# Performance work log

Measured on AMD Instinct MI355X. Metric: run time of the kernel, lower is better.

## Reference

```python
import jax, jax.numpy as jnp
import numpy as np

B, N, E = 16, 1024, 32768
HEADS, OC = 4, 8          # GATConv: out_channels = d_out // heads = 8
D_IN, A_DIM = 33, 8
DM, DO = 16, 32
EPS_LN = 1e-5


def setup_inputs() -> dict:
    key = jax.random.key(0)
    ks = jax.random.split(key, 24)
    r = lambda k, s: (0.1 * jax.random.normal(k, s)).astype(jnp.float32)
    return {
        "H": jax.random.normal(ks[0], (B, N, D_IN + A_DIM + 1), dtype=jnp.float32),
        "edge_index": jax.random.randint(ks[1], (2, E), 0, N, dtype=jnp.int32),
        "fc_s_w": r(ks[2], (DM, D_IN)), "fc_s_b": r(ks[3], (DM,)),
        "fc_a_w": r(ks[4], (DM, A_DIM)), "fc_a_b": r(ks[5], (DM,)),
        "fc_r_w": r(ks[6], (DM, 1)), "fc_r_b": r(ks[7], (DM,)),
        "fuse_q": r(ks[8], (3, DM)),
        "fuse_k_w": r(ks[9], (DM, DM)),
        "fuse_v_w": r(ks[10], (DM, DM)),
        "proj_w": r(ks[11], (DO, DM)), "proj_b": r(ks[12], (DO,)),
        "post_w": r(ks[13], (DO, DO)), "post_b": r(ks[14], (DO,)),
        "ln_g": jnp.ones((DO,), jnp.float32), "ln_b": jnp.zeros((DO,), jnp.float32),
        "gat_w": r(ks[15], (HEADS * OC, DO)),
        "att_src": r(ks[16], (HEADS, OC)),
        "att_dst": r(ks[17], (HEADS, OC)),
        "gat_b": r(ks[18], (HEADS * OC,)),
    }


def reference(H, edge_index, fc_s_w, fc_s_b, fc_a_w, fc_a_b, fc_r_w, fc_r_b,
              fuse_q, fuse_k_w, fuse_v_w, proj_w, proj_b, post_w, post_b,
              ln_g, ln_b, gat_w, att_src, att_dst, gat_b):
    # ---- ObsEmbedding: split obs | prev-action | prev-reward, embed to DM ----
    s = H[..., :D_IN]
    a = H[..., D_IN:D_IN + A_DIM]
    rr = H[..., D_IN + A_DIM:]
    tok = jnp.stack([s @ fc_s_w.T + fc_s_b,
                     a @ fc_a_w.T + fc_a_b,
                     rr @ fc_r_w.T + fc_r_b], axis=-2)            # [B,N,3,DM]
    K = tok @ fuse_k_w.T
    V = tok @ fuse_v_w.T
    attn = jnp.einsum('qd,bntd->bnqt', fuse_q, K) / jnp.sqrt(jnp.float32(DM))
    w = jax.nn.softmax(attn, axis=-1)                             # [B,N,3,3]
    fused = jnp.einsum('bnqt,bntd->bnqd', w, V).mean(-2)          # [B,N,DM]
    z = jax.nn.relu(fused) @ proj_w.T + proj_b                    # [B,N,DO]
    h = jax.nn.relu(z @ post_w.T + post_b)
    mu = h.mean(-1, keepdims=True)
    var = ((h - mu) ** 2).mean(-1, keepdims=True)
    Hn = (h - mu) / jnp.sqrt(var + EPS_LN) * ln_g + ln_b          # [B,N,DO]

    # ---- GATConv (eval mode: dropout off, add_self_loops=False) ----
    src, dst = edge_index[0], edge_index[1]
    x = (Hn @ gat_w.T).reshape(B, N, HEADS, OC)                   # [B,N,H,OC]
    a_s = (x * att_src).sum(-1)                                   # [B,N,H]
    a_d = (x * att_dst).sum(-1)
    e = jax.nn.leaky_relu(a_s[:, src] + a_d[:, dst], 0.2)         # [B,E,H]

    def per_graph(e_b, x_b):
        # scatter-softmax over incoming edges of each destination node
        m = jax.ops.segment_max(e_b, dst, num_segments=N)
        ex = jnp.exp(e_b - m[dst])
        den = jax.ops.segment_sum(ex, dst, num_segments=N)
        alpha = ex / den[dst]                                     # [E,H]
        out = jax.ops.segment_sum(alpha[:, :, None] * x_b[src], dst,
                                  num_segments=N)                 # [N,H,OC]
        A = jnp.zeros((HEADS, N, N), jnp.float32).at[:, src, dst].add(alpha.T)
        A = A / jnp.maximum(A.sum(-1, keepdims=True), 1e-9)
        return out.reshape(N, HEADS * OC) + gat_b, A

    out, A = jax.vmap(per_graph)(e, x)                            # [B,N,32], [B,H,N,N]
    return out, A
```

## Files before the change

### kernel.cpp

```cpp
#include <hip/hip_runtime.h>
#include <math.h>

namespace {

constexpr int B = 16, N = 1024, E = 32768, HEADS = 4, OC = 8;
constexpr int D_IN = 33, A_DIM = 8, DM = 16, DO = 32;
constexpr int F = D_IN + A_DIM + 1;
constexpr int CAP = 128;
constexpr int BCAP = 256;

typedef float f4 __attribute__((ext_vector_type(4)));

__device__ __forceinline__ float lrelu(float x) { return x >= 0.f ? x : 0.2f * x; }

__global__ __launch_bounds__(64) void k_node(
    const float* __restrict__ H,
    const float* __restrict__ fc_s_w, const float* __restrict__ fc_s_b,
    const float* __restrict__ fc_a_w, const float* __restrict__ fc_a_b,
    const float* __restrict__ fc_r_w, const float* __restrict__ fc_r_b,
    const float* __restrict__ fuse_q, const float* __restrict__ fuse_k_w,
    const float* __restrict__ fuse_v_w, const float* __restrict__ proj_w,
    const float* __restrict__ proj_b, const float* __restrict__ post_w,
    const float* __restrict__ post_b, const float* __restrict__ ln_g,
    const float* __restrict__ ln_b, const float* __restrict__ gat_w,
    const float* __restrict__ att_src, const float* __restrict__ att_dst,
    float* __restrict__ x_out, float* __restrict__ as_out, float* __restrict__ advi) {
  int node = blockIdx.x * blockDim.x + threadIdx.x;
  if (node >= B * N) return;

  const float* hin = H + (size_t)node * F;
  float hv[F];
#pragma unroll
  for (int i = 0; i < F; i++) hv[i] = hin[i];

  float tok[3][DM];
#pragma unroll
  for (int j = 0; j < DM; j++) {
    float acc = fc_s_b[j];
#pragma unroll
    for (int i = 0; i < D_IN; i++) acc = fmaf(hv[i], fc_s_w[j * D_IN + i], acc);
    tok[0][j] = acc;
    float acc2 = fc_a_b[j];
#pragma unroll
    for (int i = 0; i < A_DIM; i++) acc2 = fmaf(hv[D_IN + i], fc_a_w[j * A_DIM + i], acc2);
    tok[1][j] = acc2;
    tok[2][j] = fmaf(hv[F - 1], fc_r_w[j], fc_r_b[j]);
  }

  float Kf[3][DM], Vf[3][DM];
#pragma unroll
  for (int t = 0; t < 3; t++) {
#pragma unroll
    for (int j = 0; j < DM; j++) {
      float ak = 0.f, av = 0.f;
#pragma unroll
      for (int d = 0; d < DM; d++) {
        ak = fmaf(tok[t][d], fuse_k_w[j * DM + d], ak);
        av = fmaf(tok[t][d], fuse_v_w[j * DM + d], av);
      }
      Kf[t][j] = ak; Vf[t][j] = av;
    }
  }

  float wbar[3] = {0.f, 0.f, 0.f};
#pragma unroll
  for (int q = 0; q < 3; q++) {
    float att[3];
#pragma unroll
    for (int t = 0; t < 3; t++) {
      float acc = 0.f;
#pragma unroll
      for (int d = 0; d < DM; d++) acc = fmaf(fuse_q[q * DM + d], Kf[t][d], acc);
      att[t] = acc * 0.25f;
    }
    float mx = fmaxf(att[0], fmaxf(att[1], att[2]));
    float e0 = expf(att[0] - mx), e1 = expf(att[1] - mx), e2 = expf(att[2] - mx);
    float inv = 1.f / (e0 + e1 + e2);
    wbar[0] += e0 * inv; wbar[1] += e1 * inv; wbar[2] += e2 * inv;
  }

  float fused[DM];
#pragma unroll
  for (int d = 0; d < DM; d++) {
    float f = (wbar[0] * Vf[0][d] + wbar[1] * Vf[1][d] + wbar[2] * Vf[2][d]) * (1.f / 3.f);
    fused[d] = fmaxf(f, 0.f);
  }

  float z[DO];
#pragma unroll
  for (int o = 0; o < DO; o++) {
    float acc = proj_b[o];
#pragma unroll
    for (int d = 0; d < DM; d++) acc = fmaf(fused[d], proj_w[o * DM + d], acc);
    z[o] = acc;
  }

  float h2[DO]; float mu = 0.f;
#pragma unroll
  for (int o = 0; o < DO; o++) {
    float acc = post_b[o];
#pragma unroll
    for (int d = 0; d < DO; d++) acc = fmaf(z[d], post_w[o * DO + d], acc);
    acc = fmaxf(acc, 0.f);
    h2[o] = acc; mu += acc;
  }
  mu *= (1.f / DO);
  float var = 0.f;
#pragma unroll
  for (int o = 0; o < DO; o++) { float dd = h2[o] - mu; var = fmaf(dd, dd, var); }
  var *= (1.f / DO);
  float rstd = rsqrtf(var + 1e-5f);
  float Hn[DO];
#pragma unroll
  for (int o = 0; o < DO; o++) Hn[o] = fmaf((h2[o] - mu) * rstd, ln_g[o], ln_b[o]);

  float* xrow = x_out + (size_t)node * (HEADS * OC);
  f4 asv, adv;
#pragma unroll
  for (int hh = 0; hh < HEADS; hh++) {
    float as = 0.f, ad = 0.f;
#pragma unroll
    for (int oc = 0; oc < OC; oc++) {
      int k = hh * OC + oc;
      float acc = 0.f;
#pragma unroll
      for (int d = 0; d < DO; d++) acc = fmaf(Hn[d], gat_w[k * DO + d], acc);
      xrow[k] = acc;
      as = fmaf(acc, att_src[k], as);
      ad = fmaf(acc, att_dst[k], ad);
    }
    asv[hh] = as; adv[hh] = ad;
  }
  *(f4*)(as_out + (size_t)node * HEADS) = asv;
  *(f4*)(advi + (size_t)node * 8) = adv;
}

__global__ void k_fill(const int* __restrict__ ei, int* __restrict__ cnt_src,
                       int* __restrict__ cnt_dst, int* __restrict__ bkt_src,
                       int* __restrict__ bkt_dst) {
  int e = blockIdx.x * blockDim.x + threadIdx.x;
  if (e >= E) return;
  int s = ei[e], d = ei[E + e];
  int p1 = atomicAdd(&cnt_src[s], 1);
  if (p1 < BCAP) bkt_src[s * BCAP + p1] = d;
  int p2 = atomicAdd(&cnt_dst[d], 1);
  if (p2 < BCAP) bkt_dst[d * BCAP + p2] = s;
}

__global__ __launch_bounds__(256) void k_dst(
    const int* __restrict__ cnt_dst, const int* __restrict__ bkt_dst,
    const float* __restrict__ as_, float* __restrict__ advi,
    const float* __restrict__ x_, const float* __restrict__ gat_b,
    float* __restrict__ out) {
  __shared__ float s_al[4][CAP][HEADS];
  __shared__ int s_src[4][CAP];
  int w = threadIdx.x >> 6, lane = threadIdx.x & 63;
  int bd = blockIdx.x * 4 + w;
  int b = bd >> 10, dn = bd & (N - 1);
  int deg = min(cnt_dst[dn], BCAP);
  const int* list = bkt_dst + dn * BCAP;

  f4 adv = *(const f4*)(advi + (size_t)(b * N + dn) * 8);

  float sm0 = 0.f, sm1 = 0.f, sm2 = 0.f, sm3 = 0.f;
  for (int i = lane; i < deg; i += 64) {
    int s = list[i];
    f4 ap = *(const f4*)(as_ + (size_t)(b * N + s) * HEADS);
    float e0 = __expf(lrelu(ap.x + adv.x));
    float e1 = __expf(lrelu(ap.y + adv.y));
    float e2 = __expf(lrelu(ap.z + adv.z));
    float e3 = __expf(lrelu(ap.w + adv.w));
    if (i < CAP) {
      s_src[w][i] = s;
      s_al[w][i][0] = e0; s_al[w][i][1] = e1; s_al[w][i][2] = e2; s_al[w][i][3] = e3;
    }
    sm0 += e0; sm1 += e1; sm2 += e2; sm3 += e3;
  }
#pragma unroll
  for (int off = 1; off < 64; off <<= 1) {
    sm0 += __shfl_xor(sm0, off);
    sm1 += __shfl_xor(sm1, off);
    sm2 += __shfl_xor(sm2, off);
    sm3 += __shfl_xor(sm3, off);
  }
  f4 inv;
  inv.x = sm0 > 0.f ? 1.f / sm0 : 0.f;
  inv.y = sm1 > 0.f ? 1.f / sm1 : 0.f;
  inv.z = sm2 > 0.f ? 1.f / sm2 : 0.f;
  inv.w = sm3 > 0.f ? 1.f / sm3 : 0.f;
  if (lane == 0) *(f4*)(advi + (size_t)(b * N + dn) * 8 + 4) = inv;

  __syncthreads();

  int c = lane & 31;
  int h3 = c >> 3;
  float ih  = h3 == 0 ? inv.x : h3 == 1 ? inv.y : h3 == 2 ? inv.z : inv.w;
  float adh = h3 == 0 ? adv.x : h3 == 1 ? adv.y : h3 == 2 ? adv.z : adv.w;
  float acc = 0.f;
  for (int i = (lane >> 5); i < deg; i += 2) {
    float exv; int s;
    if (i < CAP) {
      exv = s_al[w][i][h3];
      s = s_src[w][i];
    } else {
      s = list[i];
      exv = __expf(lrelu(as_[(size_t)(b * N + s) * HEADS + h3] + adh));
    }
    acc = fmaf(exv, x_[(size_t)(b * N + s) * (HEADS * OC) + c], acc);
  }
  acc += __shfl_xor(acc, 32);
  if (lane < 32) out[(size_t)bd * (HEADS * OC) + c] = acc * ih + gat_b[c];
}

__global__ __launch_bounds__(256) void k_A(
    const int* __restrict__ cnt_src, const int* __restrict__ bkt_src,
    const float* __restrict__ as_, const float* __restrict__ advi,
    float* __restrict__ A) {
  __shared__ float row[HEADS][N];
  int bs = blockIdx.x;
  int s = bs & (N - 1);
  int b = bs >> 10;
  int h = threadIdx.x >> 6, lane = threadIdx.x & 63;

  f4* rowv = (f4*)row[h];
#pragma unroll
  for (int j = 0; j < 4; j++) rowv[lane + j * 64] = (f4){0.f, 0.f, 0.f, 0.f};
  __syncthreads();

  float as_h = as_[(size_t)(b * N + s) * HEADS + h];
  int deg = min(cnt_src[s], BCAP);
  const int* list = bkt_src + s * BCAP;
  float r = 0.f;
  for (int i = lane; i < deg; i += 64) {
    int d = list[i];
    const float* rec = advi + (size_t)(b * N + d) * 8;
    float a = __expf(lrelu(as_h + rec[h])) * rec[4 + h];
    atomicAdd(&row[h][d], a);
    r += a;
  }
#pragma unroll
  for (int off = 1; off < 64; off <<= 1) r += __shfl_xor(r, off);
  __syncthreads();

  float ivh = 1.f / fmaxf(r, 1e-9f);
  float* Arow = A + (((size_t)b * HEADS + h) * N + s) * N;
#pragma unroll
  for (int j = 0; j < 4; j++) {
    f4 v = rowv[lane + j * 64];
    v.x *= ivh; v.y *= ivh; v.z *= ivh; v.w *= ivh;
    __builtin_nontemporal_store(v, (f4*)Arow + lane + j * 64);
  }
}

}

extern "C" void kernel_launch(void* const* d_in, const int* in_sizes, int n_in,
                              void* d_out, int out_size, void* d_ws, size_t ws_size,
                              hipStream_t stream) {
  const float* H      = (const float*)d_in[0];
  const int*   ei     = (const int*)  d_in[1];
  const float* fc_s_w = (const float*)d_in[2];
  const float* fc_s_b = (const float*)d_in[3];
  const float* fc_a_w = (const float*)d_in[4];
  const float* fc_a_b = (const float*)d_in[5];
  const float* fc_r_w = (const float*)d_in[6];
  const float* fc_r_b = (const float*)d_in[7];
  const float* fuse_q = (const float*)d_in[8];
  const float* fuse_k_w = (const float*)d_in[9];
  const float* fuse_v_w = (const float*)d_in[10];
  const float* proj_w = (const float*)d_in[11];
  const float* proj_b = (const float*)d_in[12];
  const float* post_w = (const float*)d_in[13];
  const float* post_b = (const float*)d_in[14];
  const float* ln_g   = (const float*)d_in[15];
  const float* ln_b   = (const float*)d_in[16];
  const float* gat_w  = (const float*)d_in[17];
  const float* att_src = (const float*)d_in[18];
  const float* att_dst = (const float*)d_in[19];
  const float* gat_b  = (const float*)d_in[20];

  float* out = (float*)d_out;
  float* A   = out + (size_t)B * N * DO;

  float* ws   = (float*)d_ws;
  float* xbuf = ws;
  float* asb  = xbuf + (size_t)B * N * (HEADS * OC);
  float* advi = asb + (size_t)B * N * HEADS;
  int* ibase   = (int*)(advi + (size_t)B * N * 8);
  int* cnt_src = ibase;
  int* cnt_dst = cnt_src + N;
  int* bkt_src = cnt_dst + N;
  int* bkt_dst = bkt_src + N * BCAP;

  (void)hipMemsetAsync(cnt_src, 0, 2 * N * sizeof(int), stream);
  k_fill<<<dim3(E / 256), dim3(256), 0, stream>>>(ei, cnt_src, cnt_dst, bkt_src, bkt_dst);

  k_node<<<dim3((B * N) / 64), dim3(64), 0, stream>>>(
      H, fc_s_w, fc_s_b, fc_a_w, fc_a_b, fc_r_w, fc_r_b, fuse_q, fuse_k_w,
      fuse_v_w, proj_w, proj_b, post_w, post_b, ln_g, ln_b, gat_w, att_src,
      att_dst, xbuf, asb, advi);

  k_dst<<<dim3(B * N / 4), dim3(256), 0, stream>>>(cnt_dst, bkt_dst, asb, advi,
                                                   xbuf, gat_b, out);
  k_A<<<dim3(B * N), dim3(256), 0, stream>>>(cnt_src, bkt_src, asb, advi, A);
}
```

Before: 132.2 us.

## Merge edge-bucket fill into node kernel and fuse aggregation into A kernel

Folds the edge bucketing into the node-embedding kernel as extra blocks, which removes one launch and changes node blocks from 64 to 256 threads. The dst kernel is cut down to only computing softmax denominators. The message aggregation moves into the A-row kernel, where each block handles one (batch,node) and its four waves each aggregate one head over the incoming edges. This removes a launch and the shared-memory caching of exp values, but exp values are now recomputed and the A kernel does more work per block.

```diff
diff --git a/kernel.cpp b/kernel.cpp
--- a/kernel.cpp
+++ b/kernel.cpp
@@ -6,14 +6,17 @@
 constexpr int B = 16, N = 1024, E = 32768, HEADS = 4, OC = 8;
 constexpr int D_IN = 33, A_DIM = 8, DM = 16, DO = 32;
 constexpr int F = D_IN + A_DIM + 1;
-constexpr int CAP = 128;
 constexpr int BCAP = 256;
+constexpr int FILLB = E / 256;
 
 typedef float f4 __attribute__((ext_vector_type(4)));
 
 __device__ __forceinline__ float lrelu(float x) { return x >= 0.f ? x : 0.2f * x; }
 
-__global__ __launch_bounds__(64) void k_node(
+__global__ __launch_bounds__(256) void k_prep(
+    const int* __restrict__ ei, int* __restrict__ cnt_src,
+    int* __restrict__ cnt_dst, int* __restrict__ bkt_src,
+    int* __restrict__ bkt_dst,
     const float* __restrict__ H,
     const float* __restrict__ fc_s_w, const float* __restrict__ fc_s_b,
     const float* __restrict__ fc_a_w, const float* __restrict__ fc_a_b,
@@ -25,7 +28,16 @@
     const float* __restrict__ ln_b, const float* __restrict__ gat_w,
     const float* __restrict__ att_src, const float* __restrict__ att_dst,
     float* __restrict__ x_out, float* __restrict__ as_out, float* __restrict__ advi) {
-  int node = blockIdx.x * blockDim.x + threadIdx.x;
+  if (blockIdx.x < FILLB) {
+    int e = blockIdx.x * 256 + threadIdx.x;
+    int s = ei[e], d = ei[E + e];
+    int p1 = atomicAdd(&cnt_src[s], 1);
+    if (p1 < BCAP) bkt_src[s * BCAP + p1] = d;
+    int p2 = atomicAdd(&cnt_dst[d], 1);
+    if (p2 < BCAP) bkt_dst[d * BCAP + p2] = s;
+    return;
+  }
+  int node = (blockIdx.x - FILLB) * 256 + threadIdx.x;
   if (node >= B * N) return;
 
   const float* hin = H + (size_t)node * F;
@@ -135,25 +147,9 @@
   *(f4*)(advi + (size_t)node * 8) = adv;
 }
 
-__global__ void k_fill(const int* __restrict__ ei, int* __restrict__ cnt_src,
-                       int* __restrict__ cnt_dst, int* __restrict__ bkt_src,
-                       int* __restrict__ bkt_dst) {
-  int e = blockIdx.x * blockDim.x + threadIdx.x;
-  if (e >= E) return;
-  int s = ei[e], d = ei[E + e];
-  int p1 = atomicAdd(&cnt_src[s], 1);
-  if (p1 < BCAP) bkt_src[s * BCAP + p1] = d;
-  int p2 = atomicAdd(&cnt_dst[d], 1);
-  if (p2 < BCAP) bkt_dst[d * BCAP + p2] = s;
-}
-
-__global__ __launch_bounds__(256) void k_dst(
+__global__ __launch_bounds__(256) void k_inv(
     const int* __restrict__ cnt_dst, const int* __restrict__ bkt_dst,
-    const float* __restrict__ as_, float* __restrict__ advi,
-    const float* __restrict__ x_, const float* __restrict__ gat_b,
-    float* __restrict__ out) {
-  __shared__ float s_al[4][CAP][HEADS];
-  __shared__ int s_src[4][CAP];
+    const float* __restrict__ as_, float* __restrict__ advi) {
   int w = threadIdx.x >> 6, lane = threadIdx.x & 63;
   int bd = blockIdx.x * 4 + w;
   int b = bd >> 10, dn = bd & (N - 1);
@@ -166,15 +162,10 @@
   for (int i = lane; i < deg; i += 64) {
     int s = list[i];
     f4 ap = *(const f4*)(as_ + (size_t)(b * N + s) * HEADS);
-    float e0 = __expf(lrelu(ap.x + adv.x));
-    float e1 = __expf(lrelu(ap.y + adv.y));
-    float e2 = __expf(lrelu(ap.z + adv.z));
-    float e3 = __expf(lrelu(ap.w + adv.w));
-    if (i < CAP) {
-      s_src[w][i] = s;
-      s_al[w][i][0] = e0; s_al[w][i][1] = e1; s_al[w][i][2] = e2; s_al[w][i][3] = e3;
-    }
-    sm0 += e0; sm1 += e1; sm2 += e2; sm3 += e3;
+    sm0 += __expf(lrelu(ap.x + adv.x));
+    sm1 += __expf(lrelu(ap.y + adv.y));
+    sm2 += __expf(lrelu(ap.z + adv.z));
+    sm3 += __expf(lrelu(ap.w + adv.w));
   }
 #pragma unroll
   for (int off = 1; off < 64; off <<= 1) {
@@ -189,33 +180,14 @@
   inv.z = sm2 > 0.f ? 1.f / sm2 : 0.f;
   inv.w = sm3 > 0.f ? 1.f / sm3 : 0.f;
   if (lane == 0) *(f4*)(advi + (size_t)(b * N + dn) * 8 + 4) = inv;
-
-  __syncthreads();
-
-  int c = lane & 31;
-  int h3 = c >> 3;
-  float ih  = h3 == 0 ? inv.x : h3 == 1 ? inv.y : h3 == 2 ? inv.z : inv.w;
-  float adh = h3 == 0 ? adv.x : h3 == 1 ? adv.y : h3 == 2 ? adv.z : adv.w;
-  float acc = 0.f;
-  for (int i = (lane >> 5); i < deg; i += 2) {
-    float exv; int s;
-    if (i < CAP) {
-      exv = s_al[w][i][h3];
-      s = s_src[w][i];
-    } else {
-      s = list[i];
-      exv = __expf(lrelu(as_[(size_t)(b * N + s) * HEADS + h3] + adh));
-    }
-    acc = fmaf(exv, x_[(size_t)(b * N + s) * (HEADS * OC) + c], acc);
-  }
-  acc += __shfl_xor(acc, 32);
-  if (lane < 32) out[(size_t)bd * (HEADS * OC) + c] = acc * ih + gat_b[c];
-}
-
-__global__ __launch_bounds__(256) void k_A(
+}
+
+__global__ __launch_bounds__(256) void k_outA(
     const int* __restrict__ cnt_src, const int* __restrict__ bkt_src,
+    const int* __restrict__ cnt_dst, const int* __restrict__ bkt_dst,
     const float* __restrict__ as_, const float* __restrict__ advi,
-    float* __restrict__ A) {
+    const float* __restrict__ x_, const float* __restrict__ gat_b,
+    float* __restrict__ out, float* __restrict__ A) {
   __shared__ float row[HEADS][N];
   int bs = blockIdx.x;
   int s = bs & (N - 1);
@@ -228,11 +200,11 @@
   __syncthreads();
 
   float as_h = as_[(size_t)(b * N + s) * HEADS + h];
-  int deg = min(cnt_src[s], BCAP);
-  const int* list = bkt_src + s * BCAP;
+  int degO = min(cnt_src[s], BCAP);
+  const int* listO = bkt_src + s * BCAP;
   float r = 0.f;
-  for (int i = lane; i < deg; i += 64) {
-    int d = list[i];
+  for (int i = lane; i < degO; i += 64) {
+    int d = listO[i];
     const float* rec = advi + (size_t)(b * N + d) * 8;
     float a = __expf(lrelu(as_h + rec[h])) * rec[4 + h];
     atomicAdd(&row[h][d], a);
@@ -240,14 +212,34 @@
   }
 #pragma unroll
   for (int off = 1; off < 64; off <<= 1) r += __shfl_xor(r, off);
+
+  {
+    int degI = min(cnt_dst[s], BCAP);
+    const int* listI = bkt_dst + s * BCAP;
+    float adh = advi[(size_t)(b * N + s) * 8 + h];
+    float ivh = advi[(size_t)(b * N + s) * 8 + 4 + h];
+    int eslot = lane >> 3, cl = lane & 7, c = h * OC + cl;
+    float acc = 0.f;
+    for (int i = eslot; i < degI; i += 8) {
+      int src = listI[i];
+      float ex = __expf(lrelu(as_[(size_t)(b * N + src) * HEADS + h] + adh));
+      acc = fmaf(ex, x_[(size_t)(b * N + src) * (HEADS * OC) + c], acc);
+    }
+    acc += __shfl_xor(acc, 8);
+    acc += __shfl_xor(acc, 16);
+    acc += __shfl_xor(acc, 32);
+    if (eslot == 0)
+      out[(size_t)bs * (HEADS * OC) + c] = acc * ivh + gat_b[c];
+  }
+
   __syncthreads();
 
-  float ivh = 1.f / fmaxf(r, 1e-9f);
+  float ivr = 1.f / fmaxf(r, 1e-9f);
   float* Arow = A + (((size_t)b * HEADS + h) * N + s) * N;
 #pragma unroll
   for (int j = 0; j < 4; j++) {
     f4 v = rowv[lane + j * 64];
-    v.x *= ivh; v.y *= ivh; v.z *= ivh; v.w *= ivh;
+    v.x *= ivr; v.y *= ivr; v.z *= ivr; v.w *= ivr;
     __builtin_nontemporal_store(v, (f4*)Arow + lane + j * 64);
   }
 }
@@ -293,14 +285,14 @@
   int* bkt_dst = bkt_src + N * BCAP;
 
   (void)hipMemsetAsync(cnt_src, 0, 2 * N * sizeof(int), stream);
-  k_fill<<<dim3(E / 256), dim3(256), 0, stream>>>(ei, cnt_src, cnt_dst, bkt_src, bkt_dst);
-
-  k_node<<<dim3((B * N) / 64), dim3(64), 0, stream>>>(
+  k_prep<<<dim3(FILLB + (B * N) / 256), dim3(256), 0, stream>>>(
+      ei, cnt_src, cnt_dst, bkt_src, bkt_dst,
       H, fc_s_w, fc_s_b, fc_a_w, fc_a_b, fc_r_w, fc_r_b, fuse_q, fuse_k_w,
       fuse_v_w, proj_w, proj_b, post_w, post_b, ln_g, ln_b, gat_w, att_src,
       att_dst, xbuf, asb, advi);
 
-  k_dst<<<dim3(B * N / 4), dim3(256), 0, stream>>>(cnt_dst, bkt_dst, asb, advi,
-                                                   xbuf, gat_b, out);
-  k_A<<<dim3(B * N), dim3(256), 0, stream>>>(cnt_src, bkt_src, asb, advi, A);
-}
+  k_inv<<<dim3(B * N / 4), dim3(256), 0, stream>>>(cnt_dst, bkt_dst, asb, advi);
+
+  k_outA<<<dim3(B * N), dim3(256), 0, stream>>>(cnt_src, bkt_src, cnt_dst, bkt_dst,
+                                                asb, advi, xbuf, gat_b, out, A);
+}
```

Result: faster. 118.5 us (-10.3%).
